# Optimization experiments

Measured on AMD Instinct MI355X. Metric: run time of the kernel, lower is better.

Reference implementation:

```python
import math
import jax, jax.numpy as jnp
import numpy as np

VOCAB, D, H, L, DFF, MAXLEN, PAD = 32000, 512, 8, 6, 2048, 5000, 0
DK = D // H
EPS = 1e-5


def _positional_encoding(max_len, d_model):
    pos = np.arange(max_len, dtype=np.float32)[:, None]
    div = np.exp(np.arange(0, d_model, 2, dtype=np.float32) * (-math.log(10000.0) / d_model))
    pe = np.zeros((max_len, d_model), dtype=np.float32)
    pe[:, 0::2] = np.sin(pos * div)
    pe[:, 1::2] = np.cos(pos * div)
    return jnp.asarray(pe)


def setup_inputs() -> dict:
    key = jax.random.key(0)
    ks = jax.random.split(key, 16)
    B, S = 2, 2048
    src = jax.random.randint(ks[0], (B, S), 0, VOCAB)
    emb = jax.random.normal(ks[1], (VOCAB, D), jnp.float32) * (D ** -0.5)
    emb = emb.at[PAD].set(0.0)  # padding_idx row zeroed
    pe = _positional_encoding(MAXLEN, D)
    s = 0.02
    WQ = jax.random.normal(ks[2], (L, D, D), jnp.float32) * s
    WK = jax.random.normal(ks[3], (L, D, D), jnp.float32) * s
    WV = jax.random.normal(ks[4], (L, D, D), jnp.float32) * s
    WO = jax.random.normal(ks[5], (L, D, D), jnp.float32) * s
    W1 = jax.random.normal(ks[6], (L, D, DFF), jnp.float32) * s
    b1 = jnp.zeros((L, DFF), jnp.float32)
    W2 = jax.random.normal(ks[7], (L, DFF, D), jnp.float32) * s
    b2 = jnp.zeros((L, D), jnp.float32)
    ln1_s = jnp.ones((L, D), jnp.float32); ln1_b = jnp.zeros((L, D), jnp.float32)
    ln2_s = jnp.ones((L, D), jnp.float32); ln2_b = jnp.zeros((L, D), jnp.float32)
    fn_s = jnp.ones((D,), jnp.float32); fn_b = jnp.zeros((D,), jnp.float32)
    return dict(src=src, emb=emb, pe=pe, WQ=WQ, WK=WK, WV=WV, WO=WO,
                W1=W1, b1=b1, W2=W2, b2=b2, ln1_s=ln1_s, ln1_b=ln1_b,
                ln2_s=ln2_s, ln2_b=ln2_b, fn_s=fn_s, fn_b=fn_b)


def _layernorm(x, scale, bias):
    mu = jnp.mean(x, axis=-1, keepdims=True)
    var = jnp.mean(jnp.square(x - mu), axis=-1, keepdims=True)
    return (x - mu) * jax.lax.rsqrt(var + EPS) * scale + bias


def _encoder_forward(src, emb, pe, WQ, WK, WV, WO, W1, b1, W2, b2,
                     ln1_s, ln1_b, ln2_s, ln2_b, fn_s, fn_b):
    B, S = src.shape
    key_mask = (src != PAD)[:, None, None, :]  # [B,1,1,S] padding mask
    x = emb[src] * math.sqrt(D) + pe[:S]        # [B,S,D] (dropout=eval/off)
    for l in range(L):
        # --- pre-LN self-attention ---
        h = _layernorm(x, ln1_s[l], ln1_b[l])
        q = (h @ WQ[l]).reshape(B, S, H, DK).transpose(0, 2, 1, 3)
        k = (h @ WK[l]).reshape(B, S, H, DK).transpose(0, 2, 1, 3)
        v = (h @ WV[l]).reshape(B, S, H, DK).transpose(0, 2, 1, 3)
        scores = jnp.einsum('bhqd,bhkd->bhqk', q, k) / math.sqrt(DK)
        scores = jnp.where(key_mask, scores, -jnp.inf)
        w = jax.nn.softmax(scores, axis=-1)
        w = jnp.nan_to_num(w, nan=0.0)
        attn = jnp.einsum('bhqk,bhkd->bhqd', w, v)
        attn = attn.transpose(0, 2, 1, 3).reshape(B, S, D) @ WO[l]
        x = x + attn
        # --- pre-LN FFN ---
        h = _layernorm(x, ln2_s[l], ln2_b[l])
        h = jax.nn.relu(h @ W1[l] + b1[l]) @ W2[l] + b2[l]
        x = x + h
    return _layernorm(x, fn_s, fn_b)


def reference(src, emb, pe, WQ, WK, WV, WO, W1, b1, W2, b2,
              ln1_s, ln1_b, ln2_s, ln2_b, fn_s, fn_b):
    return _encoder_forward(src, emb, pe, WQ, WK, WV, WO, W1, b1, W2, b2,
                            ln1_s, ln1_b, ln2_s, ln2_b, fn_s, fn_b)
```

## Files before the change

### kernel.cpp

```cpp
#include <hip/hip_runtime.h>


typedef _Float16 f16;
typedef _Float16 f16x8 __attribute__((ext_vector_type(8)));
typedef _Float16 f16x4 __attribute__((ext_vector_type(4)));
typedef float    f32x4 __attribute__((ext_vector_type(4)));

#define MFMA16(a, b, c) __builtin_amdgcn_mfma_f32_16x16x32_f16((a), (b), (c), 0, 0, 0)
#define GLOAD_LDS16(GP, LP)                                        \
  __builtin_amdgcn_global_load_lds(                                \
      (const __attribute__((address_space(1))) void*)(GP),         \
      (__attribute__((address_space(3))) void*)(LP), 16, 0, 0)

__device__ inline float fast_exp2(float x) {
#if __has_builtin(__builtin_amdgcn_exp2f)
  return __builtin_amdgcn_exp2f(x);
#else
  return exp2f(x);
#endif
}

static constexpr int Dm  = 512;
static constexpr int Sx  = 2048;
static constexpr int NTOK = 4096;
static constexpr int DFFm = 2048;
static constexpr int Lc  = 6;

__global__ __launch_bounds__(256) void transpose_cvt(
    const float* __restrict__ in, f16* __restrict__ out, int R, int C,
    size_t zsi, size_t zso)
{
  __shared__ float t[32][33];
  const int z = blockIdx.z;
  const float* src = in + (size_t)z * zsi;
  f16* dst = out + (size_t)z * zso;
  const int r0 = blockIdx.y * 32, c0 = blockIdx.x * 32;
  const int tx = threadIdx.x, ty = threadIdx.y;
  #pragma unroll
  for (int i = 0; i < 4; i++)
    t[ty + i * 8][tx] = src[(size_t)(r0 + ty + i * 8) * C + c0 + tx];
  __syncthreads();
  #pragma unroll
  for (int i = 0; i < 4; i++)
    dst[(size_t)(c0 + ty + i * 8) * R + r0 + tx] = (f16)t[tx][ty + i * 8];
}

__global__ __launch_bounds__(256) void embed_k(
    const int* __restrict__ src, const float* __restrict__ emb,
    const float* __restrict__ pe, float* __restrict__ x)
{
  const int gid = blockIdx.x * 256 + threadIdx.x;
  const int token = gid >> 6;
  const int d0 = (gid & 63) << 3;
  const int s = token & (Sx - 1);
  const int tk = src[token];
  const float* e = emb + (size_t)tk * Dm + d0;
  const float* p = pe + (size_t)s * Dm + d0;
  float* o = x + (size_t)token * Dm + d0;
  const float SC = 22.627416997969522f;
  #pragma unroll
  for (int j = 0; j < 8; j++) o[j] = e[j] * SC + p[j];
}

__global__ __launch_bounds__(256) void mask_k(
    const int* __restrict__ src, float* __restrict__ mb)
{
  const int i = blockIdx.x * 256 + threadIdx.x;
  mb[i] = (src[i] != 0) ? 0.f : -3.0e38f;
}

template <typename OUT>
__global__ __launch_bounds__(256) void ln_k(
    const float* __restrict__ x, const float* __restrict__ sc,
    const float* __restrict__ bi, OUT* __restrict__ out)
{
  const int row = blockIdx.x * 4 + (threadIdx.x >> 6);
  const int l = threadIdx.x & 63;
  const float* px = x + (size_t)row * Dm + l * 8;
  float v[8];
  *(float4*)&v[0] = *(const float4*)px;
  *(float4*)&v[4] = *(const float4*)(px + 4);
  float s = 0.f;
  #pragma unroll
  for (int j = 0; j < 8; j++) s += v[j];
  #pragma unroll
  for (int m = 1; m < 64; m <<= 1) s += __shfl_xor(s, m);
  const float mu = s * (1.0f / 512.0f);
  float qv = 0.f;
  #pragma unroll
  for (int j = 0; j < 8; j++) { float d = v[j] - mu; qv += d * d; }
  #pragma unroll
  for (int m = 1; m < 64; m <<= 1) qv += __shfl_xor(qv, m);
  const float inv = rsqrtf(qv * (1.0f / 512.0f) + 1e-5f);
  float scv[8], biv[8];
  *(float4*)&scv[0] = *(const float4*)(sc + l * 8);
  *(float4*)&scv[4] = *(const float4*)(sc + l * 8 + 4);
  *(float4*)&biv[0] = *(const float4*)(bi + l * 8);
  *(float4*)&biv[4] = *(const float4*)(bi + l * 8 + 4);
  if constexpr (sizeof(OUT) == 2) {
    f16x8 o;
    #pragma unroll
    for (int j = 0; j < 8; j++) o[j] = (f16)((v[j] - mu) * inv * scv[j] + biv[j]);
    *(f16x8*)((f16*)out + (size_t)row * Dm + l * 8) = o;
  } else {
    float o[8];
    #pragma unroll
    for (int j = 0; j < 8; j++) o[j] = (v[j] - mu) * inv * scv[j] + biv[j];
    float* po = (float*)out + (size_t)row * Dm + l * 8;
    *(float4*)po = *(float4*)&o[0];
    *(float4*)(po + 4) = *(float4*)&o[4];
  }
}

template <int BN, int MODE, int N, int K, int SK>
__global__ __launch_bounds__(256) void gemm_k(
    const f16* __restrict__ A, const f16* __restrict__ Bt,
    f16* __restrict__ O0, f16* __restrict__ O1, f16* __restrict__ O2,
    float* __restrict__ xio, const float* __restrict__ bias)
{
  constexpr int BM = 128;
  constexpr int NF = BN / 32;
  constexpr int NBM = NTOK / BM;
  constexpr int NBN = N / BN;
  constexpr int NB = NBM * NBN * SK;
  __shared__ f16 lsA[2][BM * 64];
  __shared__ f16 lsB[2][BN * 64];
  const int tid = threadIdx.x;
  const int l = tid & 63, w = tid >> 6;
  const int lr = l & 15, lh = l >> 4;
  const int wm = w >> 1, wn = w & 1;
  const int bid = blockIdx.x;
  const int nid = (bid & 7) * (NB / 8) + (bid >> 3);
  const int ks = nid / (NBM * NBN);
  const int rr = nid % (NBM * NBN);
  const int bm = rr / NBN, bn = rr % NBN;

  constexpr int ACH = (BM * 64) / (256 * 8);
  constexpr int BCH = (BN * 64) / (256 * 8);
  const size_t rowA0 = (size_t)bm * BM;
  const size_t rowB0 = (size_t)bn * BN;
  const int k0 = ks * (K / SK);

  auto stage = [&](int kt, int pb) {
    #pragma unroll
    for (int i = 0; i < ACH; i++) {
      int c = i * 256 + tid, r = c >> 3, g = c & 7, gs = g ^ (r & 7);
      GLOAD_LDS16(A + (rowA0 + r) * K + k0 + kt * 64 + gs * 8, &lsA[pb][c * 8]);
    }
    #pragma unroll
    for (int i = 0; i < BCH; i++) {
      int c = i * 256 + tid, r = c >> 3, g = c & 7, gs = g ^ (r & 7);
      GLOAD_LDS16(Bt + (rowB0 + r) * K + k0 + kt * 64 + gs * 8, &lsB[pb][c * 8]);
    }
  };

  f32x4 acc[4][NF] = {};
  stage(0, 0);
  constexpr int NT = (K / SK) >> 6;
  for (int kt = 0; kt < NT; ++kt) {
    const int cur = kt & 1;
    __syncthreads();
    if (kt + 1 < NT) stage(kt + 1, cur ^ 1);
    #pragma unroll
    for (int s = 0; s < 2; s++) {
      const int gg = (s * 4 + lh) ^ (lr & 7);
      f16x8 af[4], bf[NF];
      #pragma unroll
      for (int mf = 0; mf < 4; mf++)
        af[mf] = *(const f16x8*)(&lsA[cur][(wm * 64 + mf * 16 + lr) * 64 + gg * 8]);
      #pragma unroll
      for (int nf = 0; nf < NF; nf++)
        bf[nf] = *(const f16x8*)(&lsB[cur][(wn * (BN / 2) + nf * 16 + lr) * 64 + gg * 8]);
      #pragma unroll
      for (int mf = 0; mf < 4; mf++)
        #pragma unroll
        for (int nf = 0; nf < NF; nf++)
          acc[mf][nf] = MFMA16(af[mf], bf[nf], acc[mf][nf]);
    }
  }

  #pragma unroll
  for (int mf = 0; mf < 4; mf++) {
    #pragma unroll
    for (int nf = 0; nf < NF; nf++) {
      const int token = bm * BM + wm * 64 + mf * 16 + lh * 4;
      const int ch = bn * BN + wn * (BN / 2) + nf * 16 + lr;
      if constexpr (MODE == 0) {
        const int part = ch >> 9;
        const int pch = ch & 511;
        if (part == 2) {
          f16x4 o;
          #pragma unroll
          for (int r = 0; r < 4; r++) o[r] = (f16)acc[mf][nf][r];
          const int bb = token >> 11, ss = token & (Sx - 1);
          const int scol = (ss & ~31) | (((ss >> 2) & 3) << 3) | (((ss >> 4) & 1) << 2);
          *(f16x4*)(O2 + ((size_t)((bb << 3) + (pch >> 6)) * 64 + (pch & 63)) * Sx + scol) = o;
        } else {
          f16* Oz = (part == 0) ? O0 : O1;
          #pragma unroll
          for (int r = 0; r < 4; r++)
            Oz[(size_t)(token + r) * Dm + pch] = (f16)acc[mf][nf][r];
        }
      } else {
        #pragma unroll
        for (int r = 0; r < 4; r++) {
          float v = acc[mf][nf][r];
          size_t idx = (size_t)(token + r) * N + ch;
          if constexpr (MODE == 1) {
            if constexpr (SK > 1) unsafeAtomicAdd(&xio[idx], v);
            else                  xio[idx] += v;
          } else if constexpr (MODE == 2) {
            v += bias[ch];
            O0[idx] = (f16)fmaxf(v, 0.f);
          } else {
            if (ks == 0) v += bias[ch];
            if constexpr (SK > 1) unsafeAtomicAdd(&xio[idx], v);
            else                  xio[idx] += v;
          }
        }
      }
    }
  }
}

__global__ __launch_bounds__(512) void attn_k(
    const f16* __restrict__ q, const f16* __restrict__ kk,
    const f16* __restrict__ vt, const float* __restrict__ maskb,
    f16* __restrict__ out)
{
  __shared__ f16 lsK[2][2][64 * 64];
  __shared__ f16 lsV[2][2][64 * 64];
  const int tid = threadIdx.x;
  const int l = tid & 63, w = tid >> 6;
  const int lr = l & 15, lh = l >> 4;
  const int grp = w >> 2;
  const int t256 = tid & 255;
  const int bid = blockIdx.x;
  const int nid = ((bid & 7) << 6) + (bid >> 3);
  const int bh = nid >> 5;
  const int qt = nid & 31;
  const int b = bh >> 3, h = bh & 7;

  const _Float16 QS = (_Float16)0.18033688f;
  f16x8 qf[2];
  #pragma unroll
  for (int s = 0; s < 2; s++) {
    size_t row = (size_t)(b * Sx + qt * 64 + (w & 3) * 16 + lr);
    f16x8 t = *(const f16x8*)(q + row * Dm + h * 64 + s * 32 + lh * 8);
    qf[s] = t * QS;
  }

  const f16x8 ones = {(f16)1, (f16)1, (f16)1, (f16)1,
                      (f16)1, (f16)1, (f16)1, (f16)1};
  f32x4 oacc[4] = {};
  f32x4 sumacc = {};
  float mrun = -1e30f;

  auto stage = [&](int t, int pb) {
    #pragma unroll
    for (int i = 0; i < 2; i++) {
      int c = i * 256 + t256, r = c >> 3, g = c & 7, gs = g ^ (r & 7);
      GLOAD_LDS16(kk + (size_t)(b * Sx + t * 64 + r) * Dm + h * 64 + gs * 8,
                  &lsK[grp][pb][c * 8]);
      GLOAD_LDS16(vt + (size_t)(bh * 64 + r) * Sx + t * 64 + gs * 8,
                  &lsV[grp][pb][c * 8]);
    }
  };
  stage(grp * 16, 0);

  for (int i = 0; i < 16; ++i) {
    const int t = grp * 16 + i;
    const int cur = i & 1;
    __syncthreads();
    if (i < 15) stage(t + 1, cur ^ 1);

    f32x4 sacc[4];
    #pragma unroll
    for (int kf = 0; kf < 4; kf++)
      sacc[kf] = *(const f32x4*)(maskb + b * Sx + t * 64 + kf * 16 + lh * 4);
    __builtin_amdgcn_s_setprio(1);
    #pragma unroll
    for (int s = 0; s < 2; s++) {
      const int gk = (s * 4 + lh) ^ (lr & 7);
      #pragma unroll
      for (int kf = 0; kf < 4; kf++) {
        f16x8 a = *(const f16x8*)(&lsK[grp][cur][(kf * 16 + lr) * 64 + gk * 8]);
        sacc[kf] = MFMA16(a, qf[s], sacc[kf]);
      }
    }
    __builtin_amdgcn_s_setprio(0);

    float pmax;
    {
      float t0 = fmaxf(fmaxf(sacc[0][0], sacc[0][1]), sacc[0][2]);
      float t1 = fmaxf(fmaxf(sacc[0][3], sacc[1][0]), sacc[1][1]);
      float t2 = fmaxf(fmaxf(sacc[1][2], sacc[1][3]), sacc[2][0]);
      float t3 = fmaxf(fmaxf(sacc[2][1], sacc[2][2]), sacc[2][3]);
      float t4 = fmaxf(fmaxf(sacc[3][0], sacc[3][1]), sacc[3][2]);
      float u0 = fmaxf(fmaxf(t0, t1), sacc[3][3]);
      float u1 = fmaxf(fmaxf(t2, t3), t4);
      pmax = fmaxf(u0, u1);
    }
    pmax = fmaxf(pmax, __shfl_xor(pmax, 16));
    pmax = fmaxf(pmax, __shfl_xor(pmax, 32));
    if (!__all(pmax - mrun <= 8.0f)) {
      const float mnew = fmaxf(mrun, pmax);
      const float rs = fast_exp2(mrun - mnew);
      sumacc *= rs;
      #pragma unroll
      for (int mf = 0; mf < 4; mf++) oacc[mf] *= rs;
      mrun = mnew;
    }
    #pragma unroll
    for (int kf = 0; kf < 4; kf++)
      #pragma unroll
      for (int r = 0; r < 4; r++)
        sacc[kf][r] = fast_exp2(sacc[kf][r] - mrun);
    f16x8 pa[2];
    #pragma unroll
    for (int s = 0; s < 2; s++)
      #pragma unroll
      for (int jj = 0; jj < 8; jj++)
        pa[s][jj] = (f16)sacc[2 * s + (jj >> 2)][jj & 3];
    sumacc = MFMA16(ones, pa[0], sumacc);
    sumacc = MFMA16(ones, pa[1], sumacc);

    __builtin_amdgcn_s_setprio(1);
    #pragma unroll
    for (int s = 0; s < 2; s++) {
      const int gv = (4 * s + lh) ^ (lr & 7);
      #pragma unroll
      for (int mf = 0; mf < 4; mf++) {
        f16x8 vv = *(const f16x8*)(&lsV[grp][cur][(mf * 16 + lr) * 64 + gv * 8]);
        oacc[mf] = MFMA16(vv, pa[s], oacc[mf]);
      }
    }
    __builtin_amdgcn_s_setprio(0);
  }

  const float lrun = sumacc[0];
  __syncthreads();
  float* sO  = (float*)&lsK[0][0][0];
  float* sML = (float*)&lsV[0][0][0];
  const int wl = (w & 3) * 64 + l;
  if (grp == 1) {
    #pragma unroll
    for (int mf = 0; mf < 4; mf++)
      #pragma unroll
      for (int r = 0; r < 4; r++) sO[wl * 16 + mf * 4 + r] = oacc[mf][r];
    sML[wl * 2] = mrun;
    sML[wl * 2 + 1] = lrun;
  }
  __syncthreads();
  if (grp == 0) {
    const float m1 = sML[wl * 2], l1 = sML[wl * 2 + 1];
    const float mm = fmaxf(mrun, m1);
    const float s0 = fast_exp2(mrun - mm), s1 = fast_exp2(m1 - mm);
    const float inv = 1.f / (lrun * s0 + l1 * s1);
    size_t row = (size_t)(b * Sx + qt * 64 + (w & 3) * 16 + lr);
    #pragma unroll
    for (int mf = 0; mf < 4; mf++) {
      f16x4 o;
      #pragma unroll
      for (int r = 0; r < 4; r++)
        o[r] = (f16)((oacc[mf][r] * s0 + sO[wl * 16 + mf * 4 + r] * s1) * inv);
      *(f16x4*)(out + row * Dm + h * 64 + mf * 16 + lh * 4) = o;
    }
  }
}

extern "C" void kernel_launch(void* const* d_in, const int* in_sizes, int n_in,
                              void* d_out, int out_size, void* d_ws, size_t ws_size,
                              hipStream_t stream)
{
  (void)in_sizes; (void)n_in; (void)out_size; (void)ws_size;
  const int*   src  = (const int*)d_in[0];
  const float* emb  = (const float*)d_in[1];
  const float* pe   = (const float*)d_in[2];
  const float* WQ   = (const float*)d_in[3];
  const float* WK   = (const float*)d_in[4];
  const float* WV   = (const float*)d_in[5];
  const float* WO   = (const float*)d_in[6];
  const float* W1   = (const float*)d_in[7];
  const float* b1   = (const float*)d_in[8];
  const float* W2   = (const float*)d_in[9];
  const float* b2   = (const float*)d_in[10];
  const float* ln1s = (const float*)d_in[11];
  const float* ln1b = (const float*)d_in[12];
  const float* ln2s = (const float*)d_in[13];
  const float* ln2b = (const float*)d_in[14];
  const float* fns  = (const float*)d_in[15];
  const float* fnb  = (const float*)d_in[16];

  char* ws = (char*)d_ws;
  const size_t DD = (size_t)Dm * Dm;
  const size_t DQKV = (size_t)1536 * Dm;
  const size_t DF = (size_t)Dm * DFFm;
  f16* wqkv = (f16*)(ws);
  f16* wtO  = wqkv + Lc * DQKV;
  f16* wt1  = wtO + Lc * DD;
  f16* wt2  = wt1 + Lc * DF;
  float* x  = (float*)(wt2 + Lc * DF);
  f16* hbuf = (f16*)(x + (size_t)NTOK * Dm);
  f16* qb   = hbuf + (size_t)NTOK * Dm;
  f16* kb   = qb + (size_t)NTOK * Dm;
  f16* vtb  = kb + (size_t)NTOK * Dm;
  f16* attn = vtb + (size_t)NTOK * Dm;
  f16* ff   = attn + (size_t)NTOK * Dm;
  float* maskb = (float*)(ff + (size_t)NTOK * DFFm);

  const dim3 tb(32, 8);
  transpose_cvt<<<dim3(16, 16, Lc), tb, 0, stream>>>(WQ, wqkv, Dm, Dm, DD, DQKV);
  transpose_cvt<<<dim3(16, 16, Lc), tb, 0, stream>>>(WK, wqkv + 512 * Dm, Dm, Dm, DD, DQKV);
  transpose_cvt<<<dim3(16, 16, Lc), tb, 0, stream>>>(WV, wqkv + 1024 * Dm, Dm, Dm, DD, DQKV);
  transpose_cvt<<<dim3(16, 16, Lc), tb, 0, stream>>>(WO, wtO, Dm, Dm, DD, DD);
  transpose_cvt<<<dim3(64, 16, Lc), tb, 0, stream>>>(W1, wt1, Dm, DFFm, DF, DF);
  transpose_cvt<<<dim3(16, 64, Lc), tb, 0, stream>>>(W2, wt2, DFFm, Dm, DF, DF);

  embed_k<<<1024, 256, 0, stream>>>(src, emb, pe, x);
  mask_k<<<16, 256, 0, stream>>>(src, maskb);

  for (int l = 0; l < Lc; l++) {
    const f16* wqkv_l = wqkv + (size_t)l * DQKV;
    const f16* wo = wtO + (size_t)l * DD;
    const f16* w1 = wt1 + (size_t)l * DF;
    const f16* w2 = wt2 + (size_t)l * DF;

    ln_k<f16><<<1024, 256, 0, stream>>>(x, ln1s + l * Dm, ln1b + l * Dm, hbuf);
    gemm_k<128, 0, 1536, 512, 1><<<384, 256, 0, stream>>>(
        hbuf, wqkv_l, qb, kb, vtb, nullptr, nullptr);
    attn_k<<<512, 512, 0, stream>>>(qb, kb, vtb, maskb, attn);
    gemm_k<64, 1, 512, 512, 2><<<512, 256, 0, stream>>>(
        attn, wo, nullptr, nullptr, nullptr, x, nullptr);
    ln_k<f16><<<1024, 256, 0, stream>>>(x, ln2s + l * Dm, ln2b + l * Dm, hbuf);
    gemm_k<128, 2, 2048, 512, 1><<<512, 256, 0, stream>>>(
        hbuf, w1, ff, nullptr, nullptr, nullptr, b1 + (size_t)l * DFFm);
    gemm_k<64, 3, 512, 2048, 2><<<512, 256, 0, stream>>>(
        ff, w2, nullptr, nullptr, nullptr, x, b2 + (size_t)l * Dm);
  }

  ln_k<float><<<1024, 256, 0, stream>>>(x, fns, fnb, (float*)d_out);
}
```

Before: 740.3 us.

## Double query rows per attention block and shrink QKV/FFN1 GEMM tiles

The attention kernel now handles 128 query rows per block (two 16-row fragments per wave), so each K/V tile staged in LDS feeds twice as many MFMAs, and the grid drops from 512 to 256 blocks. Softmax state, accumulators and the final two-group merge are duplicated per fragment. Separately, the QKV and FFN1 GEMMs switch from 128 to 64 row tiles with twice the blocks, aiming for better CU occupancy. The costs are higher register pressure in attention (launch bounds now request 4 waves per EU), fewer attention blocks on 256 CUs, and less weight reuse in the smaller GEMM tiles.

```diff
diff --git a/kernel.cpp b/kernel.cpp
--- a/kernel.cpp
+++ b/kernel.cpp
@@ -223,7 +223,7 @@
   }
 }
 
-__global__ __launch_bounds__(512) void attn_k(
+__global__ __launch_bounds__(512, 4) void attn_k(
     const f16* __restrict__ q, const f16* __restrict__ kk,
     const f16* __restrict__ vt, const float* __restrict__ maskb,
     f16* __restrict__ out)
@@ -233,28 +233,30 @@
   const int tid = threadIdx.x;
   const int l = tid & 63, w = tid >> 6;
   const int lr = l & 15, lh = l >> 4;
-  const int grp = w >> 2;
+  const int grp = w >> 2, wq = w & 3;
   const int t256 = tid & 255;
   const int bid = blockIdx.x;
-  const int nid = ((bid & 7) << 6) + (bid >> 3);
-  const int bh = nid >> 5;
-  const int qt = nid & 31;
+  const int nid = ((bid & 7) << 5) + (bid >> 3);
+  const int bh = nid >> 4;
+  const int qt = nid & 15;
   const int b = bh >> 3, h = bh & 7;
 
   const _Float16 QS = (_Float16)0.18033688f;
-  f16x8 qf[2];
-  #pragma unroll
-  for (int s = 0; s < 2; s++) {
-    size_t row = (size_t)(b * Sx + qt * 64 + (w & 3) * 16 + lr);
-    f16x8 t = *(const f16x8*)(q + row * Dm + h * 64 + s * 32 + lh * 8);
-    qf[s] = t * QS;
-  }
+  f16x8 qf[2][2];
+  #pragma unroll
+  for (int s = 0; s < 2; s++)
+    #pragma unroll
+    for (int j = 0; j < 2; j++) {
+      size_t row = (size_t)(b * Sx + qt * 128 + wq * 32 + j * 16 + lr);
+      f16x8 t = *(const f16x8*)(q + row * Dm + h * 64 + s * 32 + lh * 8);
+      qf[s][j] = t * QS;
+    }
 
   const f16x8 ones = {(f16)1, (f16)1, (f16)1, (f16)1,
                       (f16)1, (f16)1, (f16)1, (f16)1};
-  f32x4 oacc[4] = {};
-  f32x4 sumacc = {};
-  float mrun = -1e30f;
+  f32x4 oacc[4][2] = {};
+  f32x4 sumacc[2] = {};
+  float mrun[2] = {-1e30f, -1e30f};
 
   auto stage = [&](int t, int pb) {
     #pragma unroll
@@ -274,10 +276,13 @@
     __syncthreads();
     if (i < 15) stage(t + 1, cur ^ 1);
 
-    f32x4 sacc[4];
-    #pragma unroll
-    for (int kf = 0; kf < 4; kf++)
-      sacc[kf] = *(const f32x4*)(maskb + b * Sx + t * 64 + kf * 16 + lh * 4);
+    f32x4 sacc[4][2];
+    #pragma unroll
+    for (int kf = 0; kf < 4; kf++) {
+      f32x4 mv = *(const f32x4*)(maskb + b * Sx + t * 64 + kf * 16 + lh * 4);
+      sacc[kf][0] = mv;
+      sacc[kf][1] = mv;
+    }
     __builtin_amdgcn_s_setprio(1);
     #pragma unroll
     for (int s = 0; s < 2; s++) {
@@ -285,45 +290,49 @@
       #pragma unroll
       for (int kf = 0; kf < 4; kf++) {
         f16x8 a = *(const f16x8*)(&lsK[grp][cur][(kf * 16 + lr) * 64 + gk * 8]);
-        sacc[kf] = MFMA16(a, qf[s], sacc[kf]);
+        sacc[kf][0] = MFMA16(a, qf[s][0], sacc[kf][0]);
+        sacc[kf][1] = MFMA16(a, qf[s][1], sacc[kf][1]);
       }
     }
     __builtin_amdgcn_s_setprio(0);
 
-    float pmax;
-    {
-      float t0 = fmaxf(fmaxf(sacc[0][0], sacc[0][1]), sacc[0][2]);
-      float t1 = fmaxf(fmaxf(sacc[0][3], sacc[1][0]), sacc[1][1]);
-      float t2 = fmaxf(fmaxf(sacc[1][2], sacc[1][3]), sacc[2][0]);
-      float t3 = fmaxf(fmaxf(sacc[2][1], sacc[2][2]), sacc[2][3]);
-      float t4 = fmaxf(fmaxf(sacc[3][0], sacc[3][1]), sacc[3][2]);
-      float u0 = fmaxf(fmaxf(t0, t1), sacc[3][3]);
-      float u1 = fmaxf(fmaxf(t2, t3), t4);
-      pmax = fmaxf(u0, u1);
-    }
-    pmax = fmaxf(pmax, __shfl_xor(pmax, 16));
-    pmax = fmaxf(pmax, __shfl_xor(pmax, 32));
-    if (!__all(pmax - mrun <= 8.0f)) {
-      const float mnew = fmaxf(mrun, pmax);
-      const float rs = fast_exp2(mrun - mnew);
-      sumacc *= rs;
-      #pragma unroll
-      for (int mf = 0; mf < 4; mf++) oacc[mf] *= rs;
-      mrun = mnew;
-    }
-    #pragma unroll
-    for (int kf = 0; kf < 4; kf++)
-      #pragma unroll
-      for (int r = 0; r < 4; r++)
-        sacc[kf][r] = fast_exp2(sacc[kf][r] - mrun);
-    f16x8 pa[2];
-    #pragma unroll
-    for (int s = 0; s < 2; s++)
-      #pragma unroll
-      for (int jj = 0; jj < 8; jj++)
-        pa[s][jj] = (f16)sacc[2 * s + (jj >> 2)][jj & 3];
-    sumacc = MFMA16(ones, pa[0], sumacc);
-    sumacc = MFMA16(ones, pa[1], sumacc);
+    f16x8 pa[2][2];
+    #pragma unroll
+    for (int j = 0; j < 2; j++) {
+      float pmax;
+      {
+        float t0 = fmaxf(fmaxf(sacc[0][j][0], sacc[0][j][1]), sacc[0][j][2]);
+        float t1 = fmaxf(fmaxf(sacc[0][j][3], sacc[1][j][0]), sacc[1][j][1]);
+        float t2 = fmaxf(fmaxf(sacc[1][j][2], sacc[1][j][3]), sacc[2][j][0]);
+        float t3 = fmaxf(fmaxf(sacc[2][j][1], sacc[2][j][2]), sacc[2][j][3]);
+        float t4 = fmaxf(fmaxf(sacc[3][j][0], sacc[3][j][1]), sacc[3][j][2]);
+        float u0 = fmaxf(fmaxf(t0, t1), sacc[3][j][3]);
+        float u1 = fmaxf(fmaxf(t2, t3), t4);
+        pmax = fmaxf(u0, u1);
+      }
+      pmax = fmaxf(pmax, __shfl_xor(pmax, 16));
+      pmax = fmaxf(pmax, __shfl_xor(pmax, 32));
+      if (!__all(pmax - mrun[j] <= 8.0f)) {
+        const float mnew = fmaxf(mrun[j], pmax);
+        const float rs = fast_exp2(mrun[j] - mnew);
+        sumacc[j] *= rs;
+        #pragma unroll
+        for (int mf = 0; mf < 4; mf++) oacc[mf][j] *= rs;
+        mrun[j] = mnew;
+      }
+      #pragma unroll
+      for (int kf = 0; kf < 4; kf++)
+        #pragma unroll
+        for (int r = 0; r < 4; r++)
+          sacc[kf][j][r] = fast_exp2(sacc[kf][j][r] - mrun[j]);
+      #pragma unroll
+      for (int s = 0; s < 2; s++)
+        #pragma unroll
+        for (int jj = 0; jj < 8; jj++)
+          pa[s][j][jj] = (f16)sacc[2 * s + (jj >> 2)][j][jj & 3];
+      sumacc[j] = MFMA16(ones, pa[0][j], sumacc[j]);
+      sumacc[j] = MFMA16(ones, pa[1][j], sumacc[j]);
+    }
 
     __builtin_amdgcn_s_setprio(1);
     #pragma unroll
@@ -332,39 +341,48 @@
       #pragma unroll
       for (int mf = 0; mf < 4; mf++) {
         f16x8 vv = *(const f16x8*)(&lsV[grp][cur][(mf * 16 + lr) * 64 + gv * 8]);
-        oacc[mf] = MFMA16(vv, pa[s], oacc[mf]);
+        oacc[mf][0] = MFMA16(vv, pa[s][0], oacc[mf][0]);
+        oacc[mf][1] = MFMA16(vv, pa[s][1], oacc[mf][1]);
       }
     }
     __builtin_amdgcn_s_setprio(0);
   }
 
-  const float lrun = sumacc[0];
+  float lrun[2] = {sumacc[0][0], sumacc[1][0]};
   __syncthreads();
   float* sO  = (float*)&lsK[0][0][0];
   float* sML = (float*)&lsV[0][0][0];
-  const int wl = (w & 3) * 64 + l;
+  const int wl = wq * 64 + l;
   if (grp == 1) {
     #pragma unroll
-    for (int mf = 0; mf < 4; mf++)
-      #pragma unroll
-      for (int r = 0; r < 4; r++) sO[wl * 16 + mf * 4 + r] = oacc[mf][r];
-    sML[wl * 2] = mrun;
-    sML[wl * 2 + 1] = lrun;
+    for (int j = 0; j < 2; j++)
+      #pragma unroll
+      for (int mf = 0; mf < 4; mf++)
+        #pragma unroll
+        for (int r = 0; r < 4; r++)
+          sO[wl * 32 + j * 16 + mf * 4 + r] = oacc[mf][j][r];
+    sML[wl * 4 + 0] = mrun[0];
+    sML[wl * 4 + 1] = lrun[0];
+    sML[wl * 4 + 2] = mrun[1];
+    sML[wl * 4 + 3] = lrun[1];
   }
   __syncthreads();
   if (grp == 0) {
-    const float m1 = sML[wl * 2], l1 = sML[wl * 2 + 1];
-    const float mm = fmaxf(mrun, m1);
-    const float s0 = fast_exp2(mrun - mm), s1 = fast_exp2(m1 - mm);
-    const float inv = 1.f / (lrun * s0 + l1 * s1);
-    size_t row = (size_t)(b * Sx + qt * 64 + (w & 3) * 16 + lr);
-    #pragma unroll
-    for (int mf = 0; mf < 4; mf++) {
-      f16x4 o;
-      #pragma unroll
-      for (int r = 0; r < 4; r++)
-        o[r] = (f16)((oacc[mf][r] * s0 + sO[wl * 16 + mf * 4 + r] * s1) * inv);
-      *(f16x4*)(out + row * Dm + h * 64 + mf * 16 + lh * 4) = o;
+    #pragma unroll
+    for (int j = 0; j < 2; j++) {
+      const float m1 = sML[wl * 4 + j * 2], l1 = sML[wl * 4 + j * 2 + 1];
+      const float mm = fmaxf(mrun[j], m1);
+      const float s0 = fast_exp2(mrun[j] - mm), s1 = fast_exp2(m1 - mm);
+      const float inv = 1.f / (lrun[j] * s0 + l1 * s1);
+      size_t row = (size_t)(b * Sx + qt * 128 + wq * 32 + j * 16 + lr);
+      #pragma unroll
+      for (int mf = 0; mf < 4; mf++) {
+        f16x4 o;
+        #pragma unroll
+        for (int r = 0; r < 4; r++)
+          o[r] = (f16)((oacc[mf][j][r] * s0 + sO[wl * 32 + j * 16 + mf * 4 + r] * s1) * inv);
+        *(f16x4*)(out + row * Dm + h * 64 + mf * 16 + lh * 4) = o;
+      }
     }
   }
 }
@@ -427,13 +445,13 @@
     const f16* w2 = wt2 + (size_t)l * DF;
 
     ln_k<f16><<<1024, 256, 0, stream>>>(x, ln1s + l * Dm, ln1b + l * Dm, hbuf);
-    gemm_k<128, 0, 1536, 512, 1><<<384, 256, 0, stream>>>(
+    gemm_k<64, 0, 1536, 512, 1><<<768, 256, 0, stream>>>(
         hbuf, wqkv_l, qb, kb, vtb, nullptr, nullptr);
-    attn_k<<<512, 512, 0, stream>>>(qb, kb, vtb, maskb, attn);
+    attn_k<<<256, 512, 0, stream>>>(qb, kb, vtb, maskb, attn);
     gemm_k<64, 1, 512, 512, 2><<<512, 256, 0, stream>>>(
         attn, wo, nullptr, nullptr, nullptr, x, nullptr);
     ln_k<f16><<<1024, 256, 0, stream>>>(x, ln2s + l * Dm, ln2b + l * Dm, hbuf);
-    gemm_k<128, 2, 2048, 512, 1><<<512, 256, 0, stream>>>(
+    gemm_k<64, 2, 2048, 512, 1><<<1024, 256, 0, stream>>>(
         hbuf, w1, ff, nullptr, nullptr, nullptr, b1 + (size_t)l * DFFm);
     gemm_k<64, 3, 512, 2048, 2><<<512, 256, 0, stream>>>(
         ff, w2, nullptr, nullptr, nullptr, x, b2 + (size_t)l * Dm);
```

Result: slower. 772.7 us (+4.4%).
